# Kernel tuning notes

Hardware: AMD Instinct MI355X
Metric: run time of the kernel (lower is better)

The kernel has to match this reference:

```python
import jax, jax.numpy as jnp
import numpy as np

IOU_THRESHOLD = 0.5
EPS = 1e-7


def _make_boxes(key, n, h, w):
    k1, k2, k3, k4 = jax.random.split(key, 4)
    x1 = jax.random.uniform(k1, (n,)) * (w - 120.0)
    y1 = jax.random.uniform(k2, (n,)) * (h - 120.0)
    x2 = x1 + 20.0 + jax.random.uniform(k3, (n,)) * 100.0
    y2 = y1 + 20.0 + jax.random.uniform(k4, (n,)) * 100.0
    return jnp.stack([x1, y1, x2, y2], axis=1).astype(jnp.float32)


def setup_inputs() -> dict:
    key = jax.random.key(0)
    kd, ka, km, kt = jax.random.split(key, 4)
    N, K, H, W, MH, MW = 512, 100, 800, 800, 28, 28
    detections = _make_boxes(kd, N, H, W)[None]          # (1, N, 4) pixel coords
    annotations = _make_boxes(ka, K, H, W)[None]          # (1, K, 4) pixel coords
    masks = jax.random.uniform(km, (1, N, MH, MW, K), dtype=jnp.float32)
    masks_target = jax.random.uniform(kt, (1, K, H, W), dtype=jnp.float32)
    return {"detections": detections, "masks": masks,
            "annotations": annotations, "masks_target": masks_target}


def _overlap(a, b):
    # a: (N,4), b: (K,4) -> IoU (N,K)
    area = (b[:, 2] - b[:, 0]) * (b[:, 3] - b[:, 1])                      # (K,)
    iw = jnp.minimum(a[:, 2:3], b[None, :, 2]) - jnp.maximum(a[:, 0:1], b[None, :, 0])
    ih = jnp.minimum(a[:, 3:4], b[None, :, 3]) - jnp.maximum(a[:, 1:2], b[None, :, 1])
    iw = jnp.maximum(iw, 0.0)
    ih = jnp.maximum(ih, 0.0)
    inter = iw * ih
    ua = ((a[:, 2] - a[:, 0]) * (a[:, 3] - a[:, 1]))[:, None] + area[None, :] - inter
    return inter / jnp.maximum(ua, EPS)


def _crop_and_resize(images, boxes, box_ind, crop_size):
    # TF crop_and_resize (bilinear, extrapolation_value=0) on single-channel images.
    # images: (B, H, W); boxes: (M,4) normalized [y1,x1,y2,x2]; box_ind: (M,) int
    H, W = images.shape[1], images.shape[2]
    ch, cw = crop_size
    y1, x1, y2, x2 = boxes[:, 0], boxes[:, 1], boxes[:, 2], boxes[:, 3]
    gy = jnp.arange(ch, dtype=boxes.dtype) / (ch - 1)
    gx = jnp.arange(cw, dtype=boxes.dtype) / (cw - 1)
    in_y = (y1[:, None] + (y2 - y1)[:, None] * gy) * (H - 1)  # (M, ch)
    in_x = (x1[:, None] + (x2 - x1)[:, None] * gx) * (W - 1)  # (M, cw)
    valid_y = (in_y >= 0) & (in_y <= H - 1)
    valid_x = (in_x >= 0) & (in_x <= W - 1)
    y0 = jnp.floor(in_y)
    x0 = jnp.floor(in_x)
    yf = (in_y - y0)[:, :, None]
    xf = (in_x - x0)[:, None, :]
    y0i = jnp.clip(y0.astype(jnp.int32), 0, H - 1)
    y1i = jnp.clip(y0i + 1, 0, H - 1)
    x0i = jnp.clip(x0.astype(jnp.int32), 0, W - 1)
    x1i = jnp.clip(x0i + 1, 0, W - 1)
    b = box_ind[:, None, None]
    v00 = images[b, y0i[:, :, None], x0i[:, None, :]]
    v01 = images[b, y0i[:, :, None], x1i[:, None, :]]
    v10 = images[b, y1i[:, :, None], x0i[:, None, :]]
    v11 = images[b, y1i[:, :, None], x1i[:, None, :]]
    top = v00 + (v01 - v00) * xf
    bot = v10 + (v11 - v10) * xf
    out = top + (bot - top) * yf                                # (M, ch, cw)
    return jnp.where(valid_y[:, :, None] & valid_x[:, None, :], out, 0.0)


def reference(detections, masks, annotations, masks_target):
    d = detections[0]          # (N, 4)
    m = masks[0]               # (N, mh, mw, C)
    a = annotations[0]         # (K, 4)
    mt = masks_target[0]       # (K, H, W)
    N, mh, mw = m.shape[0], m.shape[1], m.shape[2]
    H, W = mt.shape[1], mt.shape[2]

    iou = _overlap(d, a)                               # (N, K)
    argmax_inds = jnp.argmax(iou, axis=1)              # (N,)
    max_iou = jnp.max(iou, axis=1)                     # (N,)
    valid = (max_iou >= IOU_THRESHOLD).astype(d.dtype)  # mask instead of dynamic gather

    x1, y1, x2, y2 = d[:, 0], d[:, 1], d[:, 2], d[:, 3]
    boxes = jnp.stack([y1 / H, x1 / W, y2 / H, x2 / W], axis=1)  # (N,4) normalized

    target = _crop_and_resize(mt, boxes, argmax_inds, (mh, mw))  # (N, mh, mw)
    # select the mask channel matching the assigned annotation index
    m_sel = jnp.take_along_axis(m, argmax_inds[:, None, None, None], axis=3)[..., 0]

    diff = jnp.abs(m_sel - target) * valid[:, None, None]
    n_sel = jnp.sum(valid)
    divisor = jnp.maximum(n_sel * mh * mw, 1.0)
    return jnp.sum(diff) / divisor
```

## Files before the change

### kernel.cpp

```cpp
#include <hip/hip_runtime.h>
#include <math.h>

#define N_DET 512
#define K_ANN 100
#define MH    28
#define MW    28
#define NPIX  (MH * MW)
#define IMH   800
#define IMW   800
#define IOU_THRESH 0.5f
#define EPS_F 1e-7f

__global__ __launch_bounds__(256) void maskloss_main(
    const float* __restrict__ det,
    const float* __restrict__ masks,
    const float* __restrict__ ann,
    const float* __restrict__ mt,
    float* __restrict__ ws)
{
    __shared__ float sv[256];
    __shared__ int   si[256];

    const int n   = blockIdx.x;
    const int tid = threadIdx.x;

    const float dx1 = det[n * 4 + 0];
    const float dy1 = det[n * 4 + 1];
    const float dx2 = det[n * 4 + 2];
    const float dy2 = det[n * 4 + 3];

    float best = -1.0f;
    int   bidx = 0x7FFFFFFF;
    if (tid < K_ANN) {
        const float ax1 = ann[tid * 4 + 0];
        const float ay1 = ann[tid * 4 + 1];
        const float ax2 = ann[tid * 4 + 2];
        const float ay2 = ann[tid * 4 + 3];
        const float area_k = (ax2 - ax1) * (ay2 - ay1);
        float iw = fminf(dx2, ax2) - fmaxf(dx1, ax1);
        float ih = fminf(dy2, ay2) - fmaxf(dy1, ay1);
        iw = fmaxf(iw, 0.0f);
        ih = fmaxf(ih, 0.0f);
        const float inter = iw * ih;
        const float ua = (dx2 - dx1) * (dy2 - dy1) + area_k - inter;
        best = inter / fmaxf(ua, EPS_F);
        bidx = tid;
    }

    sv[tid] = best;
    si[tid] = bidx;
    __syncthreads();
    for (int s = 128; s > 0; s >>= 1) {
        if (tid < s) {
            const float ov = sv[tid + s];
            const int   oi = si[tid + s];
            if (ov > sv[tid] || (ov == sv[tid] && oi < si[tid])) {
                sv[tid] = ov;
                si[tid] = oi;
            }
        }
        __syncthreads();
    }
    const float max_iou = sv[0];
    const int   k       = si[0];
    __syncthreads();

    if (max_iou < IOU_THRESH) return;

    const float by1 = dy1 / (float)IMH;
    const float bx1 = dx1 / (float)IMW;
    const float by2 = dy2 / (float)IMH;
    const float bx2 = dx2 / (float)IMW;

    const float* __restrict__ img = mt + (size_t)k * (IMH * IMW);
    const float* __restrict__ msk = masks + (size_t)n * NPIX * K_ANN + k;

    float local = 0.0f;
    for (int p = tid; p < NPIX; p += 256) {
        const int i = p / MW;
        const int j = p - i * MW;
        const float gy = (float)i * (1.0f / (float)(MH - 1));
        const float gx = (float)j * (1.0f / (float)(MW - 1));
        const float in_y = (by1 + (by2 - by1) * gy) * (float)(IMH - 1);
        const float in_x = (bx1 + (bx2 - bx1) * gx) * (float)(IMW - 1);
        const bool vy = (in_y >= 0.0f) && (in_y <= (float)(IMH - 1));
        const bool vx = (in_x >= 0.0f) && (in_x <= (float)(IMW - 1));
        const float y0f = floorf(in_y);
        const float x0f = floorf(in_x);
        const float yf = in_y - y0f;
        const float xf = in_x - x0f;
        int y0i = (int)y0f;
        int x0i = (int)x0f;
        y0i = min(max(y0i, 0), IMH - 1);
        x0i = min(max(x0i, 0), IMW - 1);
        const int y1i = min(y0i + 1, IMH - 1);
        const int x1i = min(x0i + 1, IMW - 1);

        const float v00 = img[y0i * IMW + x0i];
        const float v01 = img[y0i * IMW + x1i];
        const float v10 = img[y1i * IMW + x0i];
        const float v11 = img[y1i * IMW + x1i];
        const float top = v00 + (v01 - v00) * xf;
        const float bot = v10 + (v11 - v10) * xf;
        float outv = top + (bot - top) * yf;
        outv = (vy && vx) ? outv : 0.0f;

        const float msel = msk[(size_t)p * K_ANN];
        local += fabsf(msel - outv);
    }

    sv[tid] = local;
    __syncthreads();
    for (int s = 128; s > 0; s >>= 1) {
        if (tid < s) sv[tid] += sv[tid + s];
        __syncthreads();
    }
    if (tid == 0) {
        atomicAdd(&ws[0], sv[0]);
        atomicAdd(&ws[1], 1.0f);
    }
}

__global__ void maskloss_final(const float* __restrict__ ws,
                               float* __restrict__ out)
{
    const float s = ws[0];
    const float c = ws[1];
    const float divisor = fmaxf(c * (float)NPIX, 1.0f);
    out[0] = s / divisor;
}

extern "C" void kernel_launch(void* const* d_in, const int* in_sizes, int n_in,
                              void* d_out, int out_size, void* d_ws, size_t ws_size,
                              hipStream_t stream) {
    const float* det   = (const float*)d_in[0];
    const float* masks = (const float*)d_in[1];
    const float* ann   = (const float*)d_in[2];
    const float* mt    = (const float*)d_in[3];
    float* out = (float*)d_out;
    float* acc = (float*)d_ws;

    hipMemsetAsync(acc, 0, 2 * sizeof(float), stream);

    maskloss_main<<<N_DET, 256, 0, stream>>>(det, masks, ann, mt, acc);
    maskloss_final<<<1, 1, 0, stream>>>(acc, out);
}
```

Before: 350.9 us.

## Split IoU argmax and pixel loss into kernels with compacted valid-detection list

Moves the IoU/argmax step into its own 128-thread kernel, which appends each valid detection (packed index and annotation id) to a compact list with an atomic counter. A second kernel spreads each valid detection over three 256-thread blocks so the 784 pixels use nearly all threads, and blocks beyond the valid count exit early. The block reduction becomes wave shuffles plus a 4-entry shared sum. This adds a kernel launch and a grid-wide dependency between the two kernels, and the float atomic accumulation order becomes nondeterministic.

```diff
diff --git a/kernel.cpp b/kernel.cpp
--- a/kernel.cpp
+++ b/kernel.cpp
@@ -8,18 +8,18 @@
 #define NPIX  (MH * MW)
 #define IMH   800
 #define IMW   800
+#define BLOCKS_PER_DET 3
 #define IOU_THRESH 0.5f
 #define EPS_F 1e-7f
 
-__global__ __launch_bounds__(256) void maskloss_main(
+
+__global__ __launch_bounds__(128) void iou_argmax(
     const float* __restrict__ det,
-    const float* __restrict__ masks,
     const float* __restrict__ ann,
-    const float* __restrict__ mt,
-    float* __restrict__ ws)
+    int* __restrict__ wsi)
 {
-    __shared__ float sv[256];
-    __shared__ int   si[256];
+    __shared__ float sv[128];
+    __shared__ int   si[128];
 
     const int n   = blockIdx.x;
     const int tid = threadIdx.x;
@@ -50,7 +50,7 @@
     sv[tid] = best;
     si[tid] = bidx;
     __syncthreads();
-    for (int s = 128; s > 0; s >>= 1) {
+    for (int s = 64; s > 0; s >>= 1) {
         if (tid < s) {
             const float ov = sv[tid + s];
             const int   oi = si[tid + s];
@@ -61,11 +61,35 @@
         }
         __syncthreads();
     }
-    const float max_iou = sv[0];
-    const int   k       = si[0];
-    __syncthreads();
 
-    if (max_iou < IOU_THRESH) return;
+    if (tid == 0 && sv[0] >= IOU_THRESH) {
+        const int pos = atomicAdd(&wsi[0], 1);
+        wsi[2 + pos] = (n << 7) | si[0];
+    }
+}
+
+__global__ __launch_bounds__(256) void pixel_loss(
+    const float* __restrict__ det,
+    const float* __restrict__ masks,
+    const float* __restrict__ mt,
+    const int*   __restrict__ wsi,
+    float*       __restrict__ wsf)
+{
+    const int b   = blockIdx.x;
+    const int idx = b / BLOCKS_PER_DET;
+    const int rem = b - idx * BLOCKS_PER_DET;
+
+    const int count = wsi[0];
+    if (idx >= count) return;
+
+    const int packed = wsi[2 + idx];
+    const int n = packed >> 7;
+    const int k = packed & 127;
+
+    const float dx1 = det[n * 4 + 0];
+    const float dy1 = det[n * 4 + 1];
+    const float dx2 = det[n * 4 + 2];
+    const float dy2 = det[n * 4 + 3];
 
     const float by1 = dy1 / (float)IMH;
     const float bx1 = dx1 / (float)IMW;
@@ -76,7 +100,7 @@
     const float* __restrict__ msk = masks + (size_t)n * NPIX * K_ANN + k;
 
     float local = 0.0f;
-    for (int p = tid; p < NPIX; p += 256) {
+    for (int p = rem * 256 + threadIdx.x; p < NPIX; p += BLOCKS_PER_DET * 256) {
         const int i = p / MW;
         const int j = p - i * MW;
         const float gy = (float)i * (1.0f / (float)(MH - 1));
@@ -109,25 +133,25 @@
         local += fabsf(msel - outv);
     }
 
-    sv[tid] = local;
+    for (int off = 32; off > 0; off >>= 1)
+        local += __shfl_down(local, off);
+
+    __shared__ float wsum[4];
+    const int wave = threadIdx.x >> 6;
+    const int lane = threadIdx.x & 63;
+    if (lane == 0) wsum[wave] = local;
     __syncthreads();
-    for (int s = 128; s > 0; s >>= 1) {
-        if (tid < s) sv[tid] += sv[tid + s];
-        __syncthreads();
-    }
-    if (tid == 0) {
-        atomicAdd(&ws[0], sv[0]);
-        atomicAdd(&ws[1], 1.0f);
-    }
+    if (threadIdx.x == 0)
+        atomicAdd(&wsf[1], (wsum[0] + wsum[1]) + (wsum[2] + wsum[3]));
 }
 
-__global__ void maskloss_final(const float* __restrict__ ws,
+__global__ void maskloss_final(const int* __restrict__ wsi,
+                               const float* __restrict__ wsf,
                                float* __restrict__ out)
 {
-    const float s = ws[0];
-    const float c = ws[1];
+    const float c = (float)wsi[0];
     const float divisor = fmaxf(c * (float)NPIX, 1.0f);
-    out[0] = s / divisor;
+    out[0] = wsf[1] / divisor;
 }
 
 extern "C" void kernel_launch(void* const* d_in, const int* in_sizes, int n_in,
@@ -138,10 +162,12 @@
     const float* ann   = (const float*)d_in[2];
     const float* mt    = (const float*)d_in[3];
     float* out = (float*)d_out;
-    float* acc = (float*)d_ws;
+    int*   wsi = (int*)d_ws;
+    float* wsf = (float*)d_ws;
 
-    hipMemsetAsync(acc, 0, 2 * sizeof(float), stream);
+    hipMemsetAsync(d_ws, 0, 2 * sizeof(float), stream);
 
-    maskloss_main<<<N_DET, 256, 0, stream>>>(det, masks, ann, mt, acc);
-    maskloss_final<<<1, 1, 0, stream>>>(acc, out);
+    iou_argmax<<<N_DET, 128, 0, stream>>>(det, ann, wsi);
+    pixel_loss<<<N_DET * BLOCKS_PER_DET, 256, 0, stream>>>(det, masks, mt, wsi, wsf);
+    maskloss_final<<<1, 1, 0, stream>>>(wsi, wsf, out);
 }
```

Result: no change. 349.3 us (-0.5%).

## Split each detection across three blocks and replace atomics with per-block partials

Applied to the files above, without the earlier changes.

Each detection's 784 pixels are now spread over three 256-thread blocks instead of one, so every thread handles at most one pixel and no threads sit idle on a second loop pass. Each block writes its partial sum to its own workspace slot, and the first block of each detection writes a validity flag, replacing the global atomics and the memset. A 256-thread final kernel reduces the partials and flags. The block reduction is changed to wave shuffles. In exchange, the IoU argmax is recomputed three times per detection and three times as many blocks are launched.

```diff
diff --git a/kernel.cpp b/kernel.cpp
--- a/kernel.cpp
+++ b/kernel.cpp
@@ -8,20 +8,27 @@
 #define NPIX  (MH * MW)
 #define IMH   800
 #define IMW   800
+#define BLOCKS_PER_DET 3
+#define NBLK (N_DET * BLOCKS_PER_DET)
 #define IOU_THRESH 0.5f
 #define EPS_F 1e-7f
 
-__global__ __launch_bounds__(256) void maskloss_main(
+#define FLAG_BASE NBLK
+
+__global__ __launch_bounds__(256) void fused_maskloss(
     const float* __restrict__ det,
     const float* __restrict__ masks,
     const float* __restrict__ ann,
     const float* __restrict__ mt,
-    float* __restrict__ ws)
+    float* __restrict__ wsf,
+    int*   __restrict__ wsi)
 {
     __shared__ float sv[256];
     __shared__ int   si[256];
 
-    const int n   = blockIdx.x;
+    const int b   = blockIdx.x;
+    const int n   = b / BLOCKS_PER_DET;
+    const int rem = b - n * BLOCKS_PER_DET;
     const int tid = threadIdx.x;
 
     const float dx1 = det[n * 4 + 0];
@@ -65,7 +72,12 @@
     const int   k       = si[0];
     __syncthreads();
 
-    if (max_iou < IOU_THRESH) return;
+    const bool valid = (max_iou >= IOU_THRESH);
+    if (tid == 0) {
+        if (rem == 0) wsi[FLAG_BASE + n] = valid ? 1 : 0;
+        if (!valid)   wsf[b] = 0.0f;
+    }
+    if (!valid) return;
 
     const float by1 = dy1 / (float)IMH;
     const float bx1 = dx1 / (float)IMW;
@@ -76,7 +88,7 @@
     const float* __restrict__ msk = masks + (size_t)n * NPIX * K_ANN + k;
 
     float local = 0.0f;
-    for (int p = tid; p < NPIX; p += 256) {
+    for (int p = rem * 256 + tid; p < NPIX; p += BLOCKS_PER_DET * 256) {
         const int i = p / MW;
         const int j = p - i * MW;
         const float gy = (float)i * (1.0f / (float)(MH - 1));
@@ -109,25 +121,46 @@
         local += fabsf(msel - outv);
     }
 
-    sv[tid] = local;
+    for (int off = 32; off > 0; off >>= 1)
+        local += __shfl_down(local, off);
+    __shared__ float wsum[4];
+    const int wave = tid >> 6;
+    const int lane = tid & 63;
+    if (lane == 0) wsum[wave] = local;
     __syncthreads();
-    for (int s = 128; s > 0; s >>= 1) {
-        if (tid < s) sv[tid] += sv[tid + s];
-        __syncthreads();
-    }
-    if (tid == 0) {
-        atomicAdd(&ws[0], sv[0]);
-        atomicAdd(&ws[1], 1.0f);
-    }
+    if (tid == 0)
+        wsf[b] = (wsum[0] + wsum[1]) + (wsum[2] + wsum[3]);
 }
 
-__global__ void maskloss_final(const float* __restrict__ ws,
-                               float* __restrict__ out)
+__global__ __launch_bounds__(256) void maskloss_final(
+    const float* __restrict__ wsf,
+    const int*   __restrict__ wsi,
+    float* __restrict__ out)
 {
-    const float s = ws[0];
-    const float c = ws[1];
-    const float divisor = fmaxf(c * (float)NPIX, 1.0f);
-    out[0] = s / divisor;
+    const int tid = threadIdx.x;
+
+    float s = 0.0f;
+    #pragma unroll
+    for (int i = 0; i < NBLK / 256; ++i)
+        s += wsf[tid + i * 256];
+
+    int c = wsi[FLAG_BASE + tid] + wsi[FLAG_BASE + 256 + tid];
+
+    for (int off = 32; off > 0; off >>= 1) {
+        s += __shfl_down(s, off);
+        c += __shfl_down(c, off);
+    }
+    __shared__ float ssum[4];
+    __shared__ int   scnt[4];
+    const int wave = tid >> 6;
+    const int lane = tid & 63;
+    if (lane == 0) { ssum[wave] = s; scnt[wave] = c; }
+    __syncthreads();
+    if (tid == 0) {
+        const float total = (ssum[0] + ssum[1]) + (ssum[2] + ssum[3]);
+        const float cnt   = (float)(scnt[0] + scnt[1] + scnt[2] + scnt[3]);
+        out[0] = total / fmaxf(cnt * (float)NPIX, 1.0f);
+    }
 }
 
 extern "C" void kernel_launch(void* const* d_in, const int* in_sizes, int n_in,
@@ -138,10 +171,9 @@
     const float* ann   = (const float*)d_in[2];
     const float* mt    = (const float*)d_in[3];
     float* out = (float*)d_out;
-    float* acc = (float*)d_ws;
+    float* wsf = (float*)d_ws;
+    int*   wsi = (int*)d_ws;
 
-    hipMemsetAsync(acc, 0, 2 * sizeof(float), stream);
-
-    maskloss_main<<<N_DET, 256, 0, stream>>>(det, masks, ann, mt, acc);
-    maskloss_final<<<1, 1, 0, stream>>>(acc, out);
+    fused_maskloss<<<NBLK, 256, 0, stream>>>(det, masks, ann, mt, wsf, wsi);
+    maskloss_final<<<1, 256, 0, stream>>>(wsf, wsi, out);
 }
```

Result: no change. 351.0 us (+0.0%).
